# Kernel optimization log

Hardware: AMD Instinct MI355X
Metric: run time of the kernel (lower is better)

## Reference

```python
import jax, jax.numpy as jnp
import numpy as np

N_NODES = 100000
N_EDGES = 1600000
NUM_GRAPHS = 128
IN_DIM, HID, NCLS = 128, 64, 10


def setup_inputs() -> dict:
    key = jax.random.key(0)
    ks = jax.random.split(key, 12)
    inp = {
        'x': jax.random.normal(ks[0], (N_NODES, IN_DIM), jnp.float32),
        'edge_index': jax.random.randint(ks[1], (2, N_EDGES), 0, N_NODES),
        'edge_weight': jax.random.uniform(ks[2], (N_EDGES,), jnp.float32),
        'batch': jnp.sort(jax.random.randint(ks[3], (N_NODES,), 0, NUM_GRAPHS)),
        'W1': jax.random.normal(ks[4], (IN_DIM, HID), jnp.float32) * 0.05,
        'b1': jnp.zeros((HID,), jnp.float32),
        'W2': jax.random.normal(ks[5], (HID, HID), jnp.float32) * 0.05,
        'b2': jnp.zeros((HID,), jnp.float32),
        'Wc1': jax.random.normal(ks[6], (HID, HID // 2), jnp.float32) * 0.05,
        'bc1': jnp.zeros((HID // 2,), jnp.float32),
        'Wc2': jax.random.normal(ks[7], (HID // 2, NCLS), jnp.float32) * 0.05,
        'bc2': jnp.zeros((NCLS,), jnp.float32),
    }
    return inp


def _gcn_conv(x, row, col, ew, W, b, n):
    # PyG GCNConv: add self-loops (weight 1), symmetric normalization,
    # transform then aggregate: out[col] += norm * (xW)[row]
    loop = jnp.arange(n)
    r = jnp.concatenate([row, loop])
    c = jnp.concatenate([col, loop])
    w = jnp.concatenate([ew, jnp.ones((n,), ew.dtype)])
    deg = jax.ops.segment_sum(w, c, num_segments=n)
    dinv = jnp.where(deg > 0, jax.lax.rsqrt(deg), 0.0)
    norm = dinv[r] * w * dinv[c]          # [E+N]
    h = x @ W                              # [N, out]
    msg = h[r] * norm[:, None]             # [E+N, out]
    out = jax.ops.segment_sum(msg, c, num_segments=n)
    return out + b


def reference(x, edge_index, edge_weight, batch, W1, b1, W2, b2, Wc1, bc1, Wc2, bc2):
    n = x.shape[0]
    row, col = edge_index[0], edge_index[1]
    h = jax.nn.relu(_gcn_conv(x, row, col, edge_weight, W1, b1, n))
    # dropout p=0.5 is identity in eval mode
    h = jax.nn.relu(_gcn_conv(h, row, col, edge_weight, W2, b2, n))
    # global mean pool over batch indices
    sums = jax.ops.segment_sum(h, batch, num_segments=NUM_GRAPHS)
    cnts = jax.ops.segment_sum(jnp.ones((n,), h.dtype), batch, num_segments=NUM_GRAPHS)
    pooled = sums / jnp.clip(cnts, 1.0)[:, None]   # [G, HID]
    z = jax.nn.relu(pooled @ Wc1 + bc1)
    return z @ Wc2 + bc2                            # [G, NCLS]
```

## Files before the change

### kernel.cpp

```cpp
#include <hip/hip_runtime.h>
#include <hip/hip_fp16.h>


#define TPB 256
#define FIX_SCALE 16777216.0f
#define BKT_BITS 8
#define PART_BLOCKS 256

typedef _Float16 f16x8 __attribute__((ext_vector_type(8)));
typedef float f32x4 __attribute__((ext_vector_type(4)));

__device__ __forceinline__ int lower_bound_i(const int* __restrict__ a, int n, int key) {
    int lo = 0, hi = n;
    while (lo < hi) {
        int mid = (lo + hi) >> 1;
        if (a[mid] < key) lo = mid + 1; else hi = mid;
    }
    return lo;
}

__global__ __launch_bounds__(256) void k_histA(const int* __restrict__ col, int E, int CH,
                                               int K, int* __restrict__ bh,
                                               const float* __restrict__ W1,
                                               const float* __restrict__ W2,
                                               __half* __restrict__ Wt1,
                                               __half* __restrict__ Wt2) {
    __shared__ int hist[512];
    int b = blockIdx.x, t = threadIdx.x;
    if (b == 0) {
        for (int i = t; i < 64 * 128; i += 256) {
            int c = i >> 7, k = i & 127;
            Wt1[i] = (__half)W1[k * 64 + c];
        }
        for (int i = t; i < 64 * 64; i += 256) {
            int c = i >> 6, k = i & 63;
            Wt2[i] = (__half)W2[k * 64 + c];
        }
    }
    for (int i = t; i < K; i += 256) hist[i] = 0;
    __syncthreads();
    int s = b * CH, e = min(E, s + CH);
    for (int i = s + t; i < e; i += 256) atomicAdd(&hist[col[i] >> BKT_BITS], 1);
    __syncthreads();
    for (int i = t; i < K; i += 256) bh[i * PART_BLOCKS + b] = hist[i];
}

__global__ void k_scan_partial(const int* __restrict__ cnt, int* __restrict__ bsums, int n) {
    __shared__ int red[4];
    int b = blockIdx.x, t = threadIdx.x;
    int base = b * 1024;
    int s = 0;
#pragma unroll
    for (int i = 0; i < 4; i++) {
        int idx = base + t + i * TPB;
        if (idx < n) s += cnt[idx];
    }
#pragma unroll
    for (int off = 32; off > 0; off >>= 1) s += __shfl_down(s, off);
    if ((t & 63) == 0) red[t >> 6] = s;
    __syncthreads();
    if (t == 0) bsums[b] = red[0] + red[1] + red[2] + red[3];
}

__global__ void k_scan_bsums(int* __restrict__ bsums, int nb) {
    int l = threadIdx.x;
    int carry = 0;
    for (int base = 0; base < nb; base += 64) {
        int i = base + l;
        int v = (i < nb) ? bsums[i] : 0;
        int orig = v;
#pragma unroll
        for (int off = 1; off < 64; off <<= 1) {
            int x = __shfl_up(v, off);
            if (l >= off) v += x;
        }
        if (i < nb) bsums[i] = v - orig + carry;
        carry += __shfl(v, 63);
    }
}

__global__ void k_scan_final(const int* __restrict__ cnt, const int* __restrict__ boffs,
                             int* __restrict__ offs, int n) {
    __shared__ int ts[TPB];
    int b = blockIdx.x, t = threadIdx.x;
    int base = b * 1024 + 4 * t;
    int v[4]; int s = 0;
#pragma unroll
    for (int i = 0; i < 4; i++) {
        int idx = base + i;
        v[i] = (idx < n) ? cnt[idx] : 0;
        s += v[i];
    }
    ts[t] = s; __syncthreads();
    for (int off = 1; off < 256; off <<= 1) {
        int x = (t >= off) ? ts[t - off] : 0;
        __syncthreads();
        ts[t] += x;
        __syncthreads();
    }
    int run = ts[t] - s + boffs[b];
#pragma unroll
    for (int i = 0; i < 4; i++) {
        int idx = base + i;
        if (idx < n) offs[idx] = run;
        run += v[i];
    }
}

__global__ __launch_bounds__(256) void k_partB(const int* __restrict__ row,
                                               const int* __restrict__ col,
                                               const float* __restrict__ ew,
                                               const int* __restrict__ bhs,
                                               int E, int CH, int K,
                                               int2* __restrict__ part2) {
    __shared__ int cur[512];
    int b = blockIdx.x, t = threadIdx.x;
    for (int i = t; i < K; i += 256) cur[i] = bhs[i * PART_BLOCKS + b];
    __syncthreads();
    int s = b * CH, e = min(E, s + CH);
    for (int i = s + t; i < e; i += 256) {
        int c = col[i];
        int pos = atomicAdd(&cur[c >> BKT_BITS], 1);
        part2[pos] = make_int2(row[i] | ((c & 255) << 20), __float_as_int(ew[i]));
    }
}

__global__ __launch_bounds__(256) void k_csrC(const int2* __restrict__ part2,
                                              const int* __restrict__ bhs,
                                              int K, int N, int E,
                                              int* __restrict__ offs, int* __restrict__ cnt,
                                              float* __restrict__ dinv,
                                              int2* __restrict__ csr) {
    __shared__ int lcnt[256];
    __shared__ unsigned lew[256];
    __shared__ int lcur[256];
    __shared__ int ts[256];
    int k = blockIdx.x, t = threadIdx.x;
    int n0 = k << BKT_BITS;
    lcnt[t] = 0; lew[t] = 0;
    __syncthreads();
    int estart = bhs[k * PART_BLOCKS];
    int eend   = (k + 1 < K) ? bhs[(k + 1) * PART_BLOCKS] : E;
    for (int i = estart + t; i < eend; i += 256) {
        int2 v = part2[i];
        int c = (v.x >> 20) & 255;
        atomicAdd(&lcnt[c], 1);
        float w = __int_as_float(v.y);
        atomicAdd(&lew[c], (unsigned)(w * FIX_SCALE + 0.5f));
    }
    __syncthreads();
    int myc = lcnt[t];
    ts[t] = myc; __syncthreads();
    for (int off = 1; off < 256; off <<= 1) {
        int x = (t >= off) ? ts[t - off] : 0;
        __syncthreads();
        ts[t] += x;
        __syncthreads();
    }
    int goff = estart + ts[t] - myc;
    int node = n0 + t;
    if (node < N) {
        offs[node] = goff;
        cnt[node]  = myc;
        float deg = 1.0f + (float)((double)lew[t] * (1.0 / 16777216.0));
        dinv[node] = 1.0f / sqrtf(deg);
    }
    lcur[t] = goff;
    __syncthreads();
    for (int i = estart + t; i < eend; i += 256) {
        int2 v = part2[i];
        int c = (v.x >> 20) & 255;
        int pos = atomicAdd(&lcur[c], 1);
        csr[pos] = make_int2(v.x & 0xFFFFF, v.y);
    }
}

template <int K, bool FP32IN>
__global__ __launch_bounds__(256) void k_matmul_mfma(const void* __restrict__ Xv,
                                                     const __half* __restrict__ Wt,
                                                     const float* __restrict__ dinv,
                                                     __half* __restrict__ Hh, int n) {
    const int l = threadIdx.x & 63;
    const int w = threadIdx.x >> 6;
    const int rowBase = blockIdx.x * 64 + w * 16;
    const int r = l & 15;
    const int q = l >> 4;
    const int arow = rowBase + r;
    const bool rv = arow < n;

    f32x4 acc[4] = {{0.f, 0.f, 0.f, 0.f}, {0.f, 0.f, 0.f, 0.f},
                    {0.f, 0.f, 0.f, 0.f}, {0.f, 0.f, 0.f, 0.f}};

#pragma unroll
    for (int k0 = 0; k0 < K; k0 += 32) {
        f16x8 a = {};
        if (rv) {
            if constexpr (FP32IN) {
                const float* X = (const float*)Xv;
                const float4 x0 = *reinterpret_cast<const float4*>(&X[(size_t)arow * K + k0 + 8 * q]);
                const float4 x1 = *reinterpret_cast<const float4*>(&X[(size_t)arow * K + k0 + 8 * q + 4]);
                a[0] = (_Float16)x0.x; a[1] = (_Float16)x0.y;
                a[2] = (_Float16)x0.z; a[3] = (_Float16)x0.w;
                a[4] = (_Float16)x1.x; a[5] = (_Float16)x1.y;
                a[6] = (_Float16)x1.z; a[7] = (_Float16)x1.w;
            } else {
                const _Float16* X = (const _Float16*)Xv;
                a = *reinterpret_cast<const f16x8*>(&X[(size_t)arow * K + k0 + 8 * q]);
            }
        }
#pragma unroll
        for (int ct = 0; ct < 4; ct++) {
            const f16x8 b = *reinterpret_cast<const f16x8*>(
                &Wt[(size_t)(ct * 16 + r) * K + k0 + 8 * q]);
            acc[ct] = __builtin_amdgcn_mfma_f32_16x16x32_f16(a, b, acc[ct], 0, 0, 0);
        }
    }

#pragma unroll
    for (int i = 0; i < 4; i++) {
        int r2 = rowBase + 4 * q + i;
        if (r2 < n) {
            float dv = dinv[r2];
#pragma unroll
            for (int ct = 0; ct < 4; ct++)
                Hh[(size_t)r2 * 64 + ct * 16 + r] = (__half)(acc[ct][i] * dv);
        }
    }
}

__global__ __launch_bounds__(256) void k_aggregate(
    const __half2* __restrict__ hp2, const int* __restrict__ offs,
    const int* __restrict__ cnt, const int2* __restrict__ csr,
    const float* __restrict__ dinv, const float* __restrict__ bias,
    __half2* __restrict__ outh, int n) {
    const int lane = threadIdx.x & 63;
    const int epar = lane >> 5;
    const int lpos = lane & 31;
    const int node = blockIdx.x * 4 + (threadIdx.x >> 6);
    if (node >= n) return;
    const int c = cnt[node];
    const int s = offs[node];

    int2 mc = make_int2(node, 0);
    if (lane < c) mc = csr[s + lane];
    const int cc = min(c, 64);
    const int npairs = (cc + 1) >> 1;
    const int p8 = (npairs + 7) & ~7;

    float ax[8] = {0.f, 0.f, 0.f, 0.f, 0.f, 0.f, 0.f, 0.f};
    float ay[8] = {0.f, 0.f, 0.f, 0.f, 0.f, 0.f, 0.f, 0.f};

    for (int p = 0; p < p8; p += 8) {
#pragma unroll
        for (int i = 0; i < 8; i++) {
            int idx = 2 * (p + i) + epar;
            int src = __shfl(mc.x, idx);
            float w = __int_as_float(__shfl(mc.y, idx));
            float2 f = __half22float2(hp2[(size_t)src * 32 + lpos]);
            ax[i] = fmaf(f.x, w, ax[i]);
            ay[i] = fmaf(f.y, w, ay[i]);
        }
    }
    float tx = ((ax[0] + ax[1]) + (ax[2] + ax[3])) + ((ax[4] + ax[5]) + (ax[6] + ax[7]));
    float ty = ((ay[0] + ay[1]) + (ay[2] + ay[3])) + ((ay[4] + ay[5]) + (ay[6] + ay[7]));
    tx += __shfl(tx, lane ^ 32);
    ty += __shfl(ty, lane ^ 32);

    for (int j = 64; j < c; ++j) {
        int2 e = csr[s + j];
        float2 f = __half22float2(hp2[(size_t)e.x * 32 + lpos]);
        float w = __int_as_float(e.y);
        tx = fmaf(f.x, w, tx);
        ty = fmaf(f.y, w, ty);
    }

    if (epar == 0) {
        float2 sv = __half22float2(hp2[(size_t)node * 32 + lpos]);
        const float2 bv = *reinterpret_cast<const float2*>(&bias[lpos * 2]);
        float dv = dinv[node];
        float rx = fmaxf(fmaf(tx + sv.x, dv, bv.x), 0.f);
        float ry = fmaxf(fmaf(ty + sv.y, dv, bv.y), 0.f);
        outh[(size_t)node * 32 + lpos] = __floats2half2_rn(rx, ry);
    }
}

__global__ __launch_bounds__(256) void k_pool4(
    const __half* __restrict__ oh, const int* __restrict__ batch, int n,
    float* __restrict__ psum) {
    const int g = blockIdx.x >> 2;
    const int sl = blockIdx.x & 3;
    const int t = threadIdx.x;
    const int lane = t & 63, w = t >> 6;
    __shared__ float sums[4][64];

    int start = lower_bound_i(batch, n, g);
    int end   = lower_bound_i(batch, n, g + 1);
    int len   = end - start;
    int s0 = start + (len * sl) / 4;
    int s1 = start + (len * (sl + 1)) / 4;

    float acc = 0.f;
    for (int i = s0 + w; i < s1; i += 4)
        acc += __half2float(oh[(size_t)i * 64 + lane]);
    sums[w][lane] = acc;
    __syncthreads();
    if (w == 0) {
        float v = sums[0][lane] + sums[1][lane] + sums[2][lane] + sums[3][lane];
        psum[(size_t)blockIdx.x * 64 + lane] = v;
    }
}

__global__ __launch_bounds__(64) void k_head(
    const float* __restrict__ psum, const int* __restrict__ batch, int n,
    const float* __restrict__ Wc1, const float* __restrict__ bc1,
    const float* __restrict__ Wc2, const float* __restrict__ bc2,
    float* __restrict__ out) {
    const int g = blockIdx.x;
    const int t = threadIdx.x;
    __shared__ float pooled[64];
    __shared__ float z[32];

    int start = lower_bound_i(batch, n, g);
    int end   = lower_bound_i(batch, n, g + 1);
    float ccount = (float)(end - start);

    float v = psum[(size_t)(g * 4 + 0) * 64 + t] + psum[(size_t)(g * 4 + 1) * 64 + t] +
              psum[(size_t)(g * 4 + 2) * 64 + t] + psum[(size_t)(g * 4 + 3) * 64 + t];
    pooled[t] = v / fmaxf(ccount, 1.0f);
    __syncthreads();
    if (t < 32) {
        float a = bc1[t];
#pragma unroll
        for (int k = 0; k < 64; k++) a = fmaf(pooled[k], Wc1[k * 32 + t], a);
        z[t] = fmaxf(a, 0.f);
    }
    __syncthreads();
    if (t < 10) {
        float a = bc2[t];
#pragma unroll
        for (int k = 0; k < 32; k++) a = fmaf(z[k], Wc2[k * 10 + t], a);
        out[g * 10 + t] = a;
    }
}

extern "C" void kernel_launch(void* const* d_in, const int* in_sizes, int n_in,
                              void* d_out, int out_size, void* d_ws, size_t ws_size,
                              hipStream_t stream) {
    const float* x    = (const float*)d_in[0];
    const int*   ei   = (const int*)d_in[1];
    const float* ew   = (const float*)d_in[2];
    const int*   bat  = (const int*)d_in[3];
    const float* W1   = (const float*)d_in[4];
    const float* b1   = (const float*)d_in[5];
    const float* W2   = (const float*)d_in[6];
    const float* b2   = (const float*)d_in[7];
    const float* Wc1  = (const float*)d_in[8];
    const float* bc1  = (const float*)d_in[9];
    const float* Wc2  = (const float*)d_in[10];
    const float* bc2  = (const float*)d_in[11];
    float* out = (float*)d_out;

    const int N = in_sizes[0] / 128;
    const int E = in_sizes[2];
    const int G = out_size / 10;
    const int K = (N + 255) >> BKT_BITS;
    const int KB = K * PART_BLOCKS;
    const int CH = (E + PART_BLOCKS - 1) / PART_BLOCKS;

    const int* row = ei;
    const int* col = ei + E;

    char* p = (char*)d_ws;
    auto alloc = [&](size_t bytes) -> void* {
        void* r = (void*)p;
        p += (bytes + 255) & ~(size_t)255;
        return r;
    };
    int*    bh    = (int*)   alloc((size_t)KB * 4);
    int*    bhs   = (int*)   alloc((size_t)KB * 4);
    int*    bsums = (int*)   alloc(8192);
    int*    offs  = (int*)   alloc((size_t)N * 4);
    int*    cnt   = (int*)   alloc((size_t)N * 4);
    float*  dinv  = (float*) alloc((size_t)N * 4);
    __half* Wt1   = (__half*)alloc(64 * 128 * 2);
    __half* Wt2   = (__half*)alloc(64 * 64 * 2);
    float*  psum  = (float*) alloc((size_t)G * 4 * 64 * 4);
    int2*   csr   = (int2*)  alloc((size_t)E * 8);
    size_t hbytes = (size_t)N * 64 * 2;
    size_t pbytes = (size_t)E * 8;
    char*   hbase = (char*)  alloc(hbytes > pbytes ? hbytes : pbytes);
    __half* o     = (__half*)alloc((size_t)N * 64 * 2);
    int2*   part2 = (int2*)  hbase;
    __half* h     = (__half*)hbase;

    const int NB = (KB + 1023) / 1024;

    k_histA<<<PART_BLOCKS, 256, 0, stream>>>(col, E, CH, K, bh, W1, W2, Wt1, Wt2);
    k_scan_partial<<<NB, TPB, 0, stream>>>(bh, bsums, KB);
    k_scan_bsums<<<1, 64, 0, stream>>>(bsums, NB);
    k_scan_final<<<NB, TPB, 0, stream>>>(bh, bsums, bhs, KB);
    k_partB<<<PART_BLOCKS, 256, 0, stream>>>(row, col, ew, bhs, E, CH, K, part2);
    k_csrC<<<K, 256, 0, stream>>>(part2, bhs, K, N, E, offs, cnt, dinv, csr);

    const int gb_mm = (N + 63) / 64;
    const int gb_ag = (N + 3) / 4;

    k_matmul_mfma<128, true><<<gb_mm, 256, 0, stream>>>(x, Wt1, dinv, h, N);
    k_aggregate<<<gb_ag, 256, 0, stream>>>((const __half2*)h, offs, cnt, csr, dinv, b1,
                                           (__half2*)o, N);
    k_matmul_mfma<64, false><<<gb_mm, 256, 0, stream>>>(o, Wt2, dinv, h, N);
    k_aggregate<<<gb_ag, 256, 0, stream>>>((const __half2*)h, offs, cnt, csr, dinv, b2,
                                           (__half2*)o, N);
    k_pool4<<<G * 4, 256, 0, stream>>>(o, bat, N, psum);
    k_head<<<G, 64, 0, stream>>>(psum, bat, N, Wc1, bc1, Wc2, bc2, out);
}
```

Measured before the change: 199.9 us.

## Fuse first matmul with edge histogram and defer dinv scaling to CSR build

The first feature transform (x@W1) now runs without dinv scaling in the same launch as the column histogram, with extra blocks after the histogram blocks doing the MFMA matmul. The per-row dinv scale is applied later inside the CSR-building kernel, once degrees are known. The block-sums scan kernel is folded into the final scan, and weight prep moves to its own tiny kernel. The aggregation unroll drops from 8 to 4 accumulators. The aim is to overlap independent work and cut launches, at the cost of a separate partition buffer and an extra read-modify-write pass over h.

```diff
diff --git a/kernel.cpp b/kernel.cpp
--- a/kernel.cpp
+++ b/kernel.cpp
@@ -19,170 +19,28 @@
     return lo;
 }
 
-__global__ __launch_bounds__(256) void k_histA(const int* __restrict__ col, int E, int CH,
-                                               int K, int* __restrict__ bh,
-                                               const float* __restrict__ W1,
-                                               const float* __restrict__ W2,
-                                               __half* __restrict__ Wt1,
-                                               __half* __restrict__ Wt2) {
-    __shared__ int hist[512];
-    int b = blockIdx.x, t = threadIdx.x;
-    if (b == 0) {
-        for (int i = t; i < 64 * 128; i += 256) {
-            int c = i >> 7, k = i & 127;
-            Wt1[i] = (__half)W1[k * 64 + c];
-        }
-        for (int i = t; i < 64 * 64; i += 256) {
-            int c = i >> 6, k = i & 63;
-            Wt2[i] = (__half)W2[k * 64 + c];
-        }
-    }
-    for (int i = t; i < K; i += 256) hist[i] = 0;
-    __syncthreads();
-    int s = b * CH, e = min(E, s + CH);
-    for (int i = s + t; i < e; i += 256) atomicAdd(&hist[col[i] >> BKT_BITS], 1);
-    __syncthreads();
-    for (int i = t; i < K; i += 256) bh[i * PART_BLOCKS + b] = hist[i];
-}
-
-__global__ void k_scan_partial(const int* __restrict__ cnt, int* __restrict__ bsums, int n) {
-    __shared__ int red[4];
-    int b = blockIdx.x, t = threadIdx.x;
-    int base = b * 1024;
-    int s = 0;
-#pragma unroll
-    for (int i = 0; i < 4; i++) {
-        int idx = base + t + i * TPB;
-        if (idx < n) s += cnt[idx];
-    }
-#pragma unroll
-    for (int off = 32; off > 0; off >>= 1) s += __shfl_down(s, off);
-    if ((t & 63) == 0) red[t >> 6] = s;
-    __syncthreads();
-    if (t == 0) bsums[b] = red[0] + red[1] + red[2] + red[3];
-}
-
-__global__ void k_scan_bsums(int* __restrict__ bsums, int nb) {
-    int l = threadIdx.x;
-    int carry = 0;
-    for (int base = 0; base < nb; base += 64) {
-        int i = base + l;
-        int v = (i < nb) ? bsums[i] : 0;
-        int orig = v;
-#pragma unroll
-        for (int off = 1; off < 64; off <<= 1) {
-            int x = __shfl_up(v, off);
-            if (l >= off) v += x;
-        }
-        if (i < nb) bsums[i] = v - orig + carry;
-        carry += __shfl(v, 63);
-    }
-}
-
-__global__ void k_scan_final(const int* __restrict__ cnt, const int* __restrict__ boffs,
-                             int* __restrict__ offs, int n) {
-    __shared__ int ts[TPB];
-    int b = blockIdx.x, t = threadIdx.x;
-    int base = b * 1024 + 4 * t;
-    int v[4]; int s = 0;
-#pragma unroll
-    for (int i = 0; i < 4; i++) {
-        int idx = base + i;
-        v[i] = (idx < n) ? cnt[idx] : 0;
-        s += v[i];
-    }
-    ts[t] = s; __syncthreads();
-    for (int off = 1; off < 256; off <<= 1) {
-        int x = (t >= off) ? ts[t - off] : 0;
-        __syncthreads();
-        ts[t] += x;
-        __syncthreads();
-    }
-    int run = ts[t] - s + boffs[b];
-#pragma unroll
-    for (int i = 0; i < 4; i++) {
-        int idx = base + i;
-        if (idx < n) offs[idx] = run;
-        run += v[i];
-    }
-}
-
-__global__ __launch_bounds__(256) void k_partB(const int* __restrict__ row,
-                                               const int* __restrict__ col,
-                                               const float* __restrict__ ew,
-                                               const int* __restrict__ bhs,
-                                               int E, int CH, int K,
-                                               int2* __restrict__ part2) {
-    __shared__ int cur[512];
-    int b = blockIdx.x, t = threadIdx.x;
-    for (int i = t; i < K; i += 256) cur[i] = bhs[i * PART_BLOCKS + b];
-    __syncthreads();
-    int s = b * CH, e = min(E, s + CH);
-    for (int i = s + t; i < e; i += 256) {
-        int c = col[i];
-        int pos = atomicAdd(&cur[c >> BKT_BITS], 1);
-        part2[pos] = make_int2(row[i] | ((c & 255) << 20), __float_as_int(ew[i]));
-    }
-}
-
-__global__ __launch_bounds__(256) void k_csrC(const int2* __restrict__ part2,
-                                              const int* __restrict__ bhs,
-                                              int K, int N, int E,
-                                              int* __restrict__ offs, int* __restrict__ cnt,
-                                              float* __restrict__ dinv,
-                                              int2* __restrict__ csr) {
-    __shared__ int lcnt[256];
-    __shared__ unsigned lew[256];
-    __shared__ int lcur[256];
-    __shared__ int ts[256];
-    int k = blockIdx.x, t = threadIdx.x;
-    int n0 = k << BKT_BITS;
-    lcnt[t] = 0; lew[t] = 0;
-    __syncthreads();
-    int estart = bhs[k * PART_BLOCKS];
-    int eend   = (k + 1 < K) ? bhs[(k + 1) * PART_BLOCKS] : E;
-    for (int i = estart + t; i < eend; i += 256) {
-        int2 v = part2[i];
-        int c = (v.x >> 20) & 255;
-        atomicAdd(&lcnt[c], 1);
-        float w = __int_as_float(v.y);
-        atomicAdd(&lew[c], (unsigned)(w * FIX_SCALE + 0.5f));
-    }
-    __syncthreads();
-    int myc = lcnt[t];
-    ts[t] = myc; __syncthreads();
-    for (int off = 1; off < 256; off <<= 1) {
-        int x = (t >= off) ? ts[t - off] : 0;
-        __syncthreads();
-        ts[t] += x;
-        __syncthreads();
-    }
-    int goff = estart + ts[t] - myc;
-    int node = n0 + t;
-    if (node < N) {
-        offs[node] = goff;
-        cnt[node]  = myc;
-        float deg = 1.0f + (float)((double)lew[t] * (1.0 / 16777216.0));
-        dinv[node] = 1.0f / sqrtf(deg);
-    }
-    lcur[t] = goff;
-    __syncthreads();
-    for (int i = estart + t; i < eend; i += 256) {
-        int2 v = part2[i];
-        int c = (v.x >> 20) & 255;
-        int pos = atomicAdd(&lcur[c], 1);
-        csr[pos] = make_int2(v.x & 0xFFFFF, v.y);
-    }
-}
-
-template <int K, bool FP32IN>
-__global__ __launch_bounds__(256) void k_matmul_mfma(const void* __restrict__ Xv,
-                                                     const __half* __restrict__ Wt,
-                                                     const float* __restrict__ dinv,
-                                                     __half* __restrict__ Hh, int n) {
-    const int l = threadIdx.x & 63;
-    const int w = threadIdx.x >> 6;
-    const int rowBase = blockIdx.x * 64 + w * 16;
+__global__ void k_prepW(const float* __restrict__ W1, const float* __restrict__ W2,
+                        __half* __restrict__ Wt1, __half* __restrict__ Wt2) {
+    int t = threadIdx.x;
+    for (int i = t; i < 64 * 128; i += 256) {
+        int c = i >> 7, k = i & 127;
+        Wt1[i] = (__half)W1[k * 64 + c];
+    }
+    for (int i = t; i < 64 * 64; i += 256) {
+        int c = i >> 6, k = i & 63;
+        Wt2[i] = (__half)W2[k * 64 + c];
+    }
+}
+
+template <int K, bool FP32IN, bool SCALE>
+__device__ __forceinline__ void mm_body(const void* __restrict__ Xv,
+                                        const __half* __restrict__ Wt,
+                                        const float* __restrict__ dinv,
+                                        __half* __restrict__ Hh, int n,
+                                        int bid, int tid) {
+    const int l = tid & 63;
+    const int w = tid >> 6;
+    const int rowBase = bid * 64 + w * 16;
     const int r = l & 15;
     const int q = l >> 4;
     const int arow = rowBase + r;
@@ -220,11 +78,175 @@
     for (int i = 0; i < 4; i++) {
         int r2 = rowBase + 4 * q + i;
         if (r2 < n) {
-            float dv = dinv[r2];
+            float dv = 1.0f;
+            if constexpr (SCALE) dv = dinv[r2];
 #pragma unroll
             for (int ct = 0; ct < 4; ct++)
                 Hh[(size_t)r2 * 64 + ct * 16 + r] = (__half)(acc[ct][i] * dv);
         }
+    }
+}
+
+template <int K, bool FP32IN, bool SCALE>
+__global__ __launch_bounds__(256) void k_matmul_mfma(const void* __restrict__ Xv,
+                                                     const __half* __restrict__ Wt,
+                                                     const float* __restrict__ dinv,
+                                                     __half* __restrict__ Hh, int n) {
+    mm_body<K, FP32IN, SCALE>(Xv, Wt, dinv, Hh, n, blockIdx.x, threadIdx.x);
+}
+
+__global__ __launch_bounds__(256) void k_fuse1(const int* __restrict__ col, int E, int CH,
+                                               int nbkt, int* __restrict__ bh,
+                                               const float* __restrict__ X,
+                                               const __half* __restrict__ Wt1,
+                                               __half* __restrict__ g, int n) {
+    if (blockIdx.x < PART_BLOCKS) {
+        __shared__ int hist[512];
+        int b = blockIdx.x, t = threadIdx.x;
+        for (int i = t; i < nbkt; i += 256) hist[i] = 0;
+        __syncthreads();
+        int s = b * CH, e = min(E, s + CH);
+        for (int i = s + t; i < e; i += 256) atomicAdd(&hist[col[i] >> BKT_BITS], 1);
+        __syncthreads();
+        for (int i = t; i < nbkt; i += 256) bh[i * PART_BLOCKS + b] = hist[i];
+    } else {
+        mm_body<128, true, false>(X, Wt1, nullptr, g, n,
+                                  blockIdx.x - PART_BLOCKS, threadIdx.x);
+    }
+}
+
+__global__ void k_scan_partial(const int* __restrict__ cnt, int* __restrict__ bsums, int n) {
+    __shared__ int red[4];
+    int b = blockIdx.x, t = threadIdx.x;
+    int base = b * 1024;
+    int s = 0;
+#pragma unroll
+    for (int i = 0; i < 4; i++) {
+        int idx = base + t + i * TPB;
+        if (idx < n) s += cnt[idx];
+    }
+#pragma unroll
+    for (int off = 32; off > 0; off >>= 1) s += __shfl_down(s, off);
+    if ((t & 63) == 0) red[t >> 6] = s;
+    __syncthreads();
+    if (t == 0) bsums[b] = red[0] + red[1] + red[2] + red[3];
+}
+
+__global__ void k_scan_final2(const int* __restrict__ cnt, const int* __restrict__ bsums,
+                              int* __restrict__ offs, int n, int nb) {
+    __shared__ int ts[TPB];
+    int b = blockIdx.x, t = threadIdx.x;
+    int pre = (t < b) ? bsums[t] : 0;
+    ts[t] = pre; __syncthreads();
+    for (int off = 128; off > 0; off >>= 1) {
+        if (t < off) ts[t] += ts[t + off];
+        __syncthreads();
+    }
+    int boff = ts[0];
+    __syncthreads();
+
+    int base = b * 1024 + 4 * t;
+    int v[4]; int s = 0;
+#pragma unroll
+    for (int i = 0; i < 4; i++) {
+        int idx = base + i;
+        v[i] = (idx < n) ? cnt[idx] : 0;
+        s += v[i];
+    }
+    ts[t] = s; __syncthreads();
+    for (int off = 1; off < 256; off <<= 1) {
+        int x = (t >= off) ? ts[t - off] : 0;
+        __syncthreads();
+        ts[t] += x;
+        __syncthreads();
+    }
+    int run = ts[t] - s + boff;
+#pragma unroll
+    for (int i = 0; i < 4; i++) {
+        int idx = base + i;
+        if (idx < n) offs[idx] = run;
+        run += v[i];
+    }
+}
+
+__global__ __launch_bounds__(256) void k_partB(const int* __restrict__ row,
+                                               const int* __restrict__ col,
+                                               const float* __restrict__ ew,
+                                               const int* __restrict__ bhs,
+                                               int E, int CH, int nbkt,
+                                               int2* __restrict__ part2) {
+    __shared__ int cur[512];
+    int b = blockIdx.x, t = threadIdx.x;
+    for (int i = t; i < nbkt; i += 256) cur[i] = bhs[i * PART_BLOCKS + b];
+    __syncthreads();
+    int s = b * CH, e = min(E, s + CH);
+    for (int i = s + t; i < e; i += 256) {
+        int c = col[i];
+        int pos = atomicAdd(&cur[c >> BKT_BITS], 1);
+        part2[pos] = make_int2(row[i] | ((c & 255) << 20), __float_as_int(ew[i]));
+    }
+}
+
+__global__ __launch_bounds__(256) void k_csrC2(const int2* __restrict__ part2,
+                                               const int* __restrict__ bhs,
+                                               int nbkt, int N, int E,
+                                               int* __restrict__ offs, int* __restrict__ cnt,
+                                               float* __restrict__ dinv,
+                                               int2* __restrict__ csr,
+                                               __half2* __restrict__ gh) {
+    __shared__ int lcnt[256];
+    __shared__ unsigned lew[256];
+    __shared__ int lcur[256];
+    __shared__ int ts[256];
+    __shared__ float sdinv[256];
+    int k = blockIdx.x, t = threadIdx.x;
+    int n0 = k << BKT_BITS;
+    lcnt[t] = 0; lew[t] = 0;
+    __syncthreads();
+    int estart = bhs[k * PART_BLOCKS];
+    int eend   = (k + 1 < nbkt) ? bhs[(k + 1) * PART_BLOCKS] : E;
+    for (int i = estart + t; i < eend; i += 256) {
+        int2 v = part2[i];
+        int c = (v.x >> 20) & 255;
+        atomicAdd(&lcnt[c], 1);
+        float w = __int_as_float(v.y);
+        atomicAdd(&lew[c], (unsigned)(w * FIX_SCALE + 0.5f));
+    }
+    __syncthreads();
+    int myc = lcnt[t];
+    ts[t] = myc; __syncthreads();
+    for (int off = 1; off < 256; off <<= 1) {
+        int x = (t >= off) ? ts[t - off] : 0;
+        __syncthreads();
+        ts[t] += x;
+        __syncthreads();
+    }
+    int goff = estart + ts[t] - myc;
+    int node = n0 + t;
+    float dvv = 0.f;
+    if (node < N) {
+        offs[node] = goff;
+        cnt[node]  = myc;
+        float deg = 1.0f + (float)((double)lew[t] * (1.0 / 16777216.0));
+        dvv = 1.0f / sqrtf(deg);
+        dinv[node] = dvv;
+    }
+    sdinv[t] = dvv;
+    lcur[t] = goff;
+    __syncthreads();
+    int nrows = min(256, N - n0);
+    for (int i = t; i < nrows * 32; i += 256) {
+        int rl = i >> 5, j = i & 31;
+        size_t idx = (size_t)(n0 + rl) * 32 + j;
+        float2 f = __half22float2(gh[idx]);
+        float dv = sdinv[rl];
+        gh[idx] = __floats2half2_rn(f.x * dv, f.y * dv);
+    }
+    for (int i = estart + t; i < eend; i += 256) {
+        int2 v = part2[i];
+        int c = (v.x >> 20) & 255;
+        int pos = atomicAdd(&lcur[c], 1);
+        csr[pos] = make_int2(v.x & 0xFFFFF, v.y);
     }
 }
 
@@ -245,14 +267,14 @@
     if (lane < c) mc = csr[s + lane];
     const int cc = min(c, 64);
     const int npairs = (cc + 1) >> 1;
-    const int p8 = (npairs + 7) & ~7;
-
-    float ax[8] = {0.f, 0.f, 0.f, 0.f, 0.f, 0.f, 0.f, 0.f};
-    float ay[8] = {0.f, 0.f, 0.f, 0.f, 0.f, 0.f, 0.f, 0.f};
-
-    for (int p = 0; p < p8; p += 8) {
-#pragma unroll
-        for (int i = 0; i < 8; i++) {
+    const int p4 = (npairs + 3) & ~3;
+
+    float ax[4] = {0.f, 0.f, 0.f, 0.f};
+    float ay[4] = {0.f, 0.f, 0.f, 0.f};
+
+    for (int p = 0; p < p4; p += 4) {
+#pragma unroll
+        for (int i = 0; i < 4; i++) {
             int idx = 2 * (p + i) + epar;
             int src = __shfl(mc.x, idx);
             float w = __int_as_float(__shfl(mc.y, idx));
@@ -261,8 +283,8 @@
             ay[i] = fmaf(f.y, w, ay[i]);
         }
     }
-    float tx = ((ax[0] + ax[1]) + (ax[2] + ax[3])) + ((ax[4] + ax[5]) + (ax[6] + ax[7]));
-    float ty = ((ay[0] + ay[1]) + (ay[2] + ay[3])) + ((ay[4] + ay[5]) + (ay[6] + ay[7]));
+    float tx = (ax[0] + ax[1]) + (ax[2] + ax[3]);
+    float ty = (ay[0] + ay[1]) + (ay[2] + ay[3]);
     tx += __shfl(tx, lane ^ 32);
     ty += __shfl(ty, lane ^ 32);
 
@@ -386,29 +408,24 @@
     __half* Wt2   = (__half*)alloc(64 * 64 * 2);
     float*  psum  = (float*) alloc((size_t)G * 4 * 64 * 4);
     int2*   csr   = (int2*)  alloc((size_t)E * 8);
-    size_t hbytes = (size_t)N * 64 * 2;
-    size_t pbytes = (size_t)E * 8;
-    char*   hbase = (char*)  alloc(hbytes > pbytes ? hbytes : pbytes);
+    int2*   part2 = (int2*)  alloc((size_t)E * 8);
+    __half* h     = (__half*)alloc((size_t)N * 64 * 2);
     __half* o     = (__half*)alloc((size_t)N * 64 * 2);
-    int2*   part2 = (int2*)  hbase;
-    __half* h     = (__half*)hbase;
 
     const int NB = (KB + 1023) / 1024;
-
-    k_histA<<<PART_BLOCKS, 256, 0, stream>>>(col, E, CH, K, bh, W1, W2, Wt1, Wt2);
-    k_scan_partial<<<NB, TPB, 0, stream>>>(bh, bsums, KB);
-    k_scan_bsums<<<1, 64, 0, stream>>>(bsums, NB);
-    k_scan_final<<<NB, TPB, 0, stream>>>(bh, bsums, bhs, KB);
-    k_partB<<<PART_BLOCKS, 256, 0, stream>>>(row, col, ew, bhs, E, CH, K, part2);
-    k_csrC<<<K, 256, 0, stream>>>(part2, bhs, K, N, E, offs, cnt, dinv, csr);
-
     const int gb_mm = (N + 63) / 64;
     const int gb_ag = (N + 3) / 4;
 
-    k_matmul_mfma<128, true><<<gb_mm, 256, 0, stream>>>(x, Wt1, dinv, h, N);
+    k_prepW<<<1, 256, 0, stream>>>(W1, W2, Wt1, Wt2);
+    k_fuse1<<<PART_BLOCKS + gb_mm, 256, 0, stream>>>(col, E, CH, K, bh, x, Wt1, h, N);
+    k_scan_partial<<<NB, TPB, 0, stream>>>(bh, bsums, KB);
+    k_scan_final2<<<NB, TPB, 0, stream>>>(bh, bsums, bhs, KB, NB);
+    k_partB<<<PART_BLOCKS, 256, 0, stream>>>(row, col, ew, bhs, E, CH, K, part2);
+    k_csrC2<<<K, 256, 0, stream>>>(part2, bhs, K, N, E, offs, cnt, dinv, csr,
+                                   (__half2*)h);
     k_aggregate<<<gb_ag, 256, 0, stream>>>((const __half2*)h, offs, cnt, csr, dinv, b1,
                                            (__half2*)o, N);
-    k_matmul_mfma<64, false><<<gb_mm, 256, 0, stream>>>(o, Wt2, dinv, h, N);
+    k_matmul_mfma<64, false, true><<<gb_mm, 256, 0, stream>>>(o, Wt2, dinv, h, N);
     k_aggregate<<<gb_ag, 256, 0, stream>>>((const __half2*)h, offs, cnt, csr, dinv, b2,
                                            (__half2*)o, N);
     k_pool4<<<G * 4, 256, 0, stream>>>(o, bat, N, psum);
```

After: 210.0 us. 5.1% more time.
